# Kernel optimization log

Hardware: AMD Instinct MI355X
Metric: run time of the kernel (lower is better)

The kernel has to match this reference:

```python
import jax, jax.numpy as jnp
import numpy as np

CHUNKS = 4      # number of segments along in_features
QMAX = 127.0    # int8 symmetric fake quantization
EPS = 1e-8


def fake_quantize(t):
    """Per-tensor symmetric int8 fake quantization with amax scaling (STE-friendly)."""
    amax = jnp.max(jnp.abs(t))
    scale = jnp.maximum(amax / QMAX, EPS)
    q = jnp.clip(jnp.round(t / scale), -QMAX, QMAX) * scale
    # straight-through estimator: identity gradient through the quantizer
    return t + jax.lax.stop_gradient(q - t)


def setup_inputs() -> dict:
    key = jax.random.key(0)
    kx, kw = jax.random.split(key)
    N, K, O = 4096, 4096, 4096  # tokens (B*S), in_features, out_features
    x = jax.random.normal(kx, (N, K), dtype=jnp.float32)
    weight = jax.random.normal(kw, (O, K), dtype=jnp.float32)
    return {"x": x, "weight": weight}


def reference(x, weight):
    # seg_mode='input': split x and weight along in_features into CHUNKS equal chunks,
    # fake-quantize each chunk independently (per-chunk amax scale), run per-chunk
    # GEMMs y_i = fq(x_i) @ fq(w_i)^T and sum over chunks. No bias in 'input' mode.
    N, K = x.shape
    O = weight.shape[0]
    cs = K // CHUNKS
    xc = x.reshape(N, CHUNKS, cs)       # [N, C, cs]
    wc = weight.reshape(O, CHUNKS, cs)  # [O, C, cs]
    fq_chunks = jax.vmap(fake_quantize, in_axes=1, out_axes=1)  # independent amax per chunk
    xq = fq_chunks(xc)
    wq = fq_chunks(wc)
    # sum of per-chunk matmuls == contraction over (chunk, within-chunk) axes
    return jnp.einsum('nck,ock->no', xq, wq)
```

## Files before the change

### kernel.cpp

```cpp
#include <hip/hip_runtime.h>
#include <hip/hip_bf16.h>


constexpr int NDIM = 4096;
constexpr int TOTAL4 = (NDIM * NDIM) / 4;

typedef int i32x4 __attribute__((ext_vector_type(4)));

__global__ __launch_bounds__(256) void amax_kernel(
    const float* __restrict__ x, const float* __restrict__ w,
    unsigned int* __restrict__ amax) {
  const int t = threadIdx.x;
  const int c = blockIdx.x & 3;
  float mx = 0.f, mw = 0.f;
  const float4* x4 = (const float4*)x;
  const float4* w4 = (const float4*)w;
  const int stride = 1024 * 256;
  for (int i = blockIdx.x * 256 + t; i < TOTAL4; i += stride) {
    float4 v = x4[i];
    mx = fmaxf(mx, fmaxf(fmaxf(fabsf(v.x), fabsf(v.y)),
                         fmaxf(fabsf(v.z), fabsf(v.w))));
    float4 u = w4[i];
    mw = fmaxf(mw, fmaxf(fmaxf(fabsf(u.x), fabsf(u.y)),
                         fmaxf(fabsf(u.z), fabsf(u.w))));
  }
  __shared__ float r0[256], r1[256];
  r0[t] = mx; r1[t] = mw;
  __syncthreads();
  for (int off = 128; off; off >>= 1) {
    if (t < off) {
      r0[t] = fmaxf(r0[t], r0[t + off]);
      r1[t] = fmaxf(r1[t], r1[t + off]);
    }
    __syncthreads();
  }
  if (t == 0) {
    atomicMax(&amax[c],     __float_as_uint(r0[0]));
    atomicMax(&amax[4 + c], __float_as_uint(r1[0]));
  }
}

__device__ __forceinline__ signed char quant1(float v, float s) {
  float r = rintf(v / s);
  r = fminf(fmaxf(r, -127.f), 127.f);
  return (signed char)(int)r;
}

__global__ __launch_bounds__(256) void quant_kernel(
    const float* __restrict__ x, const float* __restrict__ w,
    const unsigned int* __restrict__ amax,
    signed char* __restrict__ qx, signed char* __restrict__ qw) {
  const int t = threadIdx.x;
  const int c = blockIdx.x & 3;
  const float sx = fmaxf(__uint_as_float(amax[c])     / 127.0f, 1e-8f);
  const float sw = fmaxf(__uint_as_float(amax[4 + c]) / 127.0f, 1e-8f);
  const float4* x4 = (const float4*)x;
  const float4* w4 = (const float4*)w;
  char4* qx4 = (char4*)qx;
  char4* qw4 = (char4*)qw;
  const int stride = 1024 * 256;
  for (int i = blockIdx.x * 256 + t; i < TOTAL4; i += stride) {
    float4 v = x4[i];
    char4 q;
    q.x = quant1(v.x, sx); q.y = quant1(v.y, sx);
    q.z = quant1(v.z, sx); q.w = quant1(v.w, sx);
    qx4[i] = q;
    float4 u = w4[i];
    char4 p;
    p.x = quant1(u.x, sw); p.y = quant1(u.y, sw);
    p.z = quant1(u.z, sw); p.w = quant1(u.w, sw);
    qw4[i] = p;
  }
}

__device__ __forceinline__ void async16(const void* g, void* l) {
  __builtin_amdgcn_global_load_lds(
      (const __attribute__((address_space(1))) void*)g,
      (__attribute__((address_space(3))) void*)l, 16, 0, 0);
}

__global__ __launch_bounds__(256, 2) void gemm_i8_kernel(
    const signed char* __restrict__ qx, const signed char* __restrict__ qw,
    const unsigned int* __restrict__ amax, float* __restrict__ out) {
  __shared__ __align__(1024) signed char lds_a[3][8192];
  __shared__ __align__(1024) signed char lds_b[3][8192];

  const int t = threadIdx.x;
  const int lane = t & 63;
  const int wave = t >> 6;
  const int brow = blockIdx.y * 128;
  const int bcol = blockIdx.x * 128;
  const int wr = wave >> 1;
  const int wc = wave & 1;

  const float s0 = fmaxf(__uint_as_float(amax[0]) / 127.0f, 1e-8f) *
                   fmaxf(__uint_as_float(amax[4]) / 127.0f, 1e-8f);
  const float s1 = fmaxf(__uint_as_float(amax[1]) / 127.0f, 1e-8f) *
                   fmaxf(__uint_as_float(amax[5]) / 127.0f, 1e-8f);
  const float s2 = fmaxf(__uint_as_float(amax[2]) / 127.0f, 1e-8f) *
                   fmaxf(__uint_as_float(amax[6]) / 127.0f, 1e-8f);
  const float s3 = fmaxf(__uint_as_float(amax[3]) / 127.0f, 1e-8f) *
                   fmaxf(__uint_as_float(amax[7]) / 127.0f, 1e-8f);
  asm volatile("s_waitcnt vmcnt(0)" ::: "memory");
  __builtin_amdgcn_sched_barrier(0);

  const int ar0 = wave * 16 + (lane >> 2);
  const int ar1 = ar0 + 64;
  const int sl = lane & 3;
  const signed char* gax0 = qx + (size_t)(brow + ar0) * NDIM + ((sl ^ ((ar0 >> 1) & 3)) << 4);
  const signed char* gax1 = qx + (size_t)(brow + ar1) * NDIM + ((sl ^ ((ar1 >> 1) & 3)) << 4);
  const signed char* gbx0 = qw + (size_t)(bcol + ar0) * NDIM + ((sl ^ ((ar0 >> 1) & 3)) << 4);
  const signed char* gbx1 = qw + (size_t)(bcol + ar1) * NDIM + ((sl ^ ((ar1 >> 1) & 3)) << 4);
  const int ldsoff = wave * 1024;

  const int ra = wr * 64 + (lane & 15);
  const int rb = wc * 64 + (lane & 15);
  const int kg = lane >> 4;
  const int offa = ra * 64 + ((kg ^ ((ra >> 1) & 3)) << 4);
  const int offb = rb * 64 + ((kg ^ ((rb >> 1) & 3)) << 4);

#define STAGE(BUFOFF, T)                                         \
  do {                                                           \
    const int kt_ = (T) * 64;                                    \
    signed char* la_ = &lds_a[0][0] + (BUFOFF) + ldsoff;         \
    signed char* lb_ = &lds_b[0][0] + (BUFOFF) + ldsoff;         \
    async16(gax0 + kt_, la_);                                    \
    async16(gax1 + kt_, la_ + 4096);                             \
    async16(gbx0 + kt_, lb_);                                    \
    async16(gbx1 + kt_, lb_ + 4096);                             \
  } while (0)

  STAGE(0, 0);
  STAGE(8192, 1);
  STAGE(16384, 2);

  i32x4 iacc[4][4];
  float facc[4][4][4];
#pragma unroll
  for (int m = 0; m < 4; ++m)
#pragma unroll
    for (int n = 0; n < 4; ++n) {
      iacc[m][n] = i32x4{0, 0, 0, 0};
#pragma unroll
      for (int j = 0; j < 4; ++j) facc[m][n][j] = 0.f;
    }

#define COMPUTE(BUFOFF)                                                 \
  do {                                                                  \
    const signed char* la_ = &lds_a[0][0] + (BUFOFF);                   \
    const signed char* lb_ = &lds_b[0][0] + (BUFOFF);                   \
    i32x4 av[4], bv[4];                                                 \
    _Pragma("unroll")                                                   \
    for (int m = 0; m < 4; ++m)                                         \
      av[m] = *(const i32x4*)&la_[offa + m * 1024];                     \
    _Pragma("unroll")                                                   \
    for (int n = 0; n < 4; ++n)                                         \
      bv[n] = *(const i32x4*)&lb_[offb + n * 1024];                     \
    __builtin_amdgcn_s_setprio(1);                                      \
    _Pragma("unroll")                                                   \
    for (int m = 0; m < 4; ++m)                                         \
      _Pragma("unroll")                                                 \
      for (int n = 0; n < 4; ++n)                                       \
        iacc[m][n] = __builtin_amdgcn_mfma_i32_16x16x64_i8(             \
            av[m], bv[n], iacc[m][n], 0, 0, 0);                         \
    __builtin_amdgcn_s_setprio(0);                                      \
  } while (0)

#define FOLD(S)                                                         \
  do {                                                                  \
    _Pragma("unroll")                                                   \
    for (int m = 0; m < 4; ++m)                                         \
      _Pragma("unroll")                                                 \
      for (int n = 0; n < 4; ++n) {                                     \
        _Pragma("unroll")                                               \
        for (int j = 0; j < 4; ++j) facc[m][n][j] += (S) * (float)iacc[m][n][j]; \
        iacc[m][n] = i32x4{0, 0, 0, 0};                                 \
      }                                                                 \
  } while (0)

#define WAITV(N) \
  asm volatile("s_waitcnt vmcnt(" #N ")" ::: "memory"); \
  __builtin_amdgcn_sched_barrier(0)
#define WAITL \
  asm volatile("s_waitcnt lgkmcnt(0)" ::: "memory"); \
  __builtin_amdgcn_sched_barrier(0)
#define BAR \
  __builtin_amdgcn_s_barrier(); \
  __builtin_amdgcn_sched_barrier(0)

  int bufoff = 0;
#pragma unroll 1
  for (int tt = 0; tt < 62; ++tt) {
    WAITV(8); BAR;
    COMPUTE(bufoff);
    WAITL; BAR;
    if (tt < 61) STAGE(bufoff, tt + 3);
    if ((tt & 15) == 15) {
      const int ci = tt >> 4;
      FOLD(ci == 0 ? s0 : ci == 1 ? s1 : s2);
    }
    bufoff = (bufoff == 16384) ? 0 : bufoff + 8192;
  }
  WAITV(4); BAR;
  COMPUTE(16384);
  WAITL; BAR;
  WAITV(0); BAR;
  COMPUTE(0);
  FOLD(s3);

  const int orow = brow + wr * 64 + (lane >> 4) * 4;
  const int ocol = bcol + wc * 64 + (lane & 15);
#pragma unroll
  for (int m = 0; m < 4; ++m)
#pragma unroll
    for (int n = 0; n < 4; ++n)
#pragma unroll
      for (int j = 0; j < 4; ++j)
        out[(size_t)(orow + m * 16 + j) * NDIM + (ocol + n * 16)] = facc[m][n][j];
#undef STAGE
#undef COMPUTE
#undef FOLD
#undef WAITV
#undef WAITL
#undef BAR
}

extern "C" void kernel_launch(void* const* d_in, const int* in_sizes, int n_in,
                              void* d_out, int out_size, void* d_ws, size_t ws_size,
                              hipStream_t stream) {
  const float* x = (const float*)d_in[0];
  const float* w = (const float*)d_in[1];
  float* out = (float*)d_out;

  unsigned int* amax = (unsigned int*)d_ws;
  signed char* qx = (signed char*)d_ws + 256;
  signed char* qw = qx + (size_t)NDIM * NDIM;

  hipMemsetAsync(d_ws, 0, 256, stream);
  amax_kernel<<<1024, 256, 0, stream>>>(x, w, amax);
  quant_kernel<<<1024, 256, 0, stream>>>(x, w, amax, qx, qw);
  dim3 grid(NDIM / 128, NDIM / 128);
  gemm_i8_kernel<<<grid, 256, 0, stream>>>(qx, qw, amax, out);
}
```

Baseline: 163.9 us.

## Use K=128 tiles with double buffering instead of K=64 triple buffering

The int8 GEMM main loop now stages 128-wide K tiles, eight async global-to-LDS loads per thread per stage, into two 16 KB buffers per operand instead of three 8 KB ones. Each compute step issues two halves of MFMAs over the wider tile, halving the number of barrier and wait rounds. The LDS swizzle is reworked to an 8-way XOR for the 128-byte rows. In exchange, prefetch depth drops from three stages to two, which may expose more global latency. Per-thread load counts and vmcnt thresholds also change.

```diff
diff --git a/kernel.cpp b/kernel.cpp
--- a/kernel.cpp
+++ b/kernel.cpp
@@ -82,8 +82,8 @@
 __global__ __launch_bounds__(256, 2) void gemm_i8_kernel(
     const signed char* __restrict__ qx, const signed char* __restrict__ qw,
     const unsigned int* __restrict__ amax, float* __restrict__ out) {
-  __shared__ __align__(1024) signed char lds_a[3][8192];
-  __shared__ __align__(1024) signed char lds_b[3][8192];
+  __shared__ __align__(1024) signed char lds_a[2][16384];
+  __shared__ __align__(1024) signed char lds_b[2][16384];
 
   const int t = threadIdx.x;
   const int lane = t & 63;
@@ -104,35 +104,35 @@
   asm volatile("s_waitcnt vmcnt(0)" ::: "memory");
   __builtin_amdgcn_sched_barrier(0);
 
-  const int ar0 = wave * 16 + (lane >> 2);
-  const int ar1 = ar0 + 64;
-  const int sl = lane & 3;
-  const signed char* gax0 = qx + (size_t)(brow + ar0) * NDIM + ((sl ^ ((ar0 >> 1) & 3)) << 4);
-  const signed char* gax1 = qx + (size_t)(brow + ar1) * NDIM + ((sl ^ ((ar1 >> 1) & 3)) << 4);
-  const signed char* gbx0 = qw + (size_t)(bcol + ar0) * NDIM + ((sl ^ ((ar0 >> 1) & 3)) << 4);
-  const signed char* gbx1 = qw + (size_t)(bcol + ar1) * NDIM + ((sl ^ ((ar1 >> 1) & 3)) << 4);
-  const int ldsoff = wave * 1024;
-
-  const int ra = wr * 64 + (lane & 15);
-  const int rb = wc * 64 + (lane & 15);
+  const int srow = t >> 3;
+  const int scol = (((t & 7) ^ (srow & 7)) << 4);
+  const signed char* gA = qx + (size_t)(brow + srow) * NDIM + scol;
+  const signed char* gB = qw + (size_t)(bcol + srow) * NDIM + scol;
+  signed char* laW = &lds_a[0][0] + wave * 1024;
+  signed char* lbW = &lds_b[0][0] + wave * 1024;
+
   const int kg = lane >> 4;
-  const int offa = ra * 64 + ((kg ^ ((ra >> 1) & 3)) << 4);
-  const int offb = rb * 64 + ((kg ^ ((rb >> 1) & 3)) << 4);
-
-#define STAGE(BUFOFF, T)                                         \
-  do {                                                           \
-    const int kt_ = (T) * 64;                                    \
-    signed char* la_ = &lds_a[0][0] + (BUFOFF) + ldsoff;         \
-    signed char* lb_ = &lds_b[0][0] + (BUFOFF) + ldsoff;         \
-    async16(gax0 + kt_, la_);                                    \
-    async16(gax1 + kt_, la_ + 4096);                             \
-    async16(gbx0 + kt_, lb_);                                    \
-    async16(gbx1 + kt_, lb_ + 4096);                             \
+  const int l7 = lane & 7;
+  const int sk0 = ((kg) ^ l7) << 4;
+  const int sk1 = ((4 + kg) ^ l7) << 4;
+  const int rba = (wr * 64 + (lane & 15)) * 128;
+  const int rbb = (wc * 64 + (lane & 15)) * 128;
+
+#define STAGE(BUFOFF, T)                                              \
+  do {                                                                \
+    const size_t kt_ = (size_t)(T) * 128;                             \
+    async16(gA + kt_,                  laW + (BUFOFF));               \
+    async16(gA + kt_ + 32u * NDIM,     laW + (BUFOFF) + 4096);        \
+    async16(gA + kt_ + 64u * NDIM,     laW + (BUFOFF) + 8192);        \
+    async16(gA + kt_ + 96u * NDIM,     laW + (BUFOFF) + 12288);       \
+    async16(gB + kt_,                  lbW + (BUFOFF));               \
+    async16(gB + kt_ + 32u * NDIM,     lbW + (BUFOFF) + 4096);        \
+    async16(gB + kt_ + 64u * NDIM,     lbW + (BUFOFF) + 8192);        \
+    async16(gB + kt_ + 96u * NDIM,     lbW + (BUFOFF) + 12288);       \
   } while (0)
 
   STAGE(0, 0);
-  STAGE(8192, 1);
-  STAGE(16384, 2);
+  STAGE(16384, 1);
 
   i32x4 iacc[4][4];
   float facc[4][4][4];
@@ -145,17 +145,15 @@
       for (int j = 0; j < 4; ++j) facc[m][n][j] = 0.f;
     }
 
-#define COMPUTE(BUFOFF)                                                 \
+#define HALF(LA, LB, SK)                                                \
   do {                                                                  \
-    const signed char* la_ = &lds_a[0][0] + (BUFOFF);                   \
-    const signed char* lb_ = &lds_b[0][0] + (BUFOFF);                   \
     i32x4 av[4], bv[4];                                                 \
     _Pragma("unroll")                                                   \
     for (int m = 0; m < 4; ++m)                                         \
-      av[m] = *(const i32x4*)&la_[offa + m * 1024];                     \
+      av[m] = *(const i32x4*)&(LA)[rba + m * 2048 + (SK)];              \
     _Pragma("unroll")                                                   \
     for (int n = 0; n < 4; ++n)                                         \
-      bv[n] = *(const i32x4*)&lb_[offb + n * 1024];                     \
+      bv[n] = *(const i32x4*)&(LB)[rbb + n * 2048 + (SK)];              \
     __builtin_amdgcn_s_setprio(1);                                      \
     _Pragma("unroll")                                                   \
     for (int m = 0; m < 4; ++m)                                         \
@@ -164,6 +162,14 @@
         iacc[m][n] = __builtin_amdgcn_mfma_i32_16x16x64_i8(             \
             av[m], bv[n], iacc[m][n], 0, 0, 0);                         \
     __builtin_amdgcn_s_setprio(0);                                      \
+  } while (0)
+
+#define COMPUTE(BUFOFF)                                                 \
+  do {                                                                  \
+    const signed char* la_ = &lds_a[0][0] + (BUFOFF);                   \
+    const signed char* lb_ = &lds_b[0][0] + (BUFOFF);                   \
+    HALF(la_, lb_, sk0);                                                \
+    HALF(la_, lb_, sk1);                                                \
   } while (0)
 
 #define FOLD(S)                                                         \
@@ -188,24 +194,26 @@
   __builtin_amdgcn_s_barrier(); \
   __builtin_amdgcn_sched_barrier(0)
 
-  int bufoff = 0;
 #pragma unroll 1
-  for (int tt = 0; tt < 62; ++tt) {
+  for (int it = 0; it < 15; ++it) {
     WAITV(8); BAR;
-    COMPUTE(bufoff);
+    COMPUTE(0);
     WAITL; BAR;
-    if (tt < 61) STAGE(bufoff, tt + 3);
-    if ((tt & 15) == 15) {
-      const int ci = tt >> 4;
+    STAGE(0, 2 * it + 2);
+    WAITV(8); BAR;
+    COMPUTE(16384);
+    WAITL; BAR;
+    STAGE(16384, 2 * it + 3);
+    if ((it & 3) == 3) {
+      const int ci = it >> 2;
       FOLD(ci == 0 ? s0 : ci == 1 ? s1 : s2);
     }
-    bufoff = (bufoff == 16384) ? 0 : bufoff + 8192;
-  }
-  WAITV(4); BAR;
-  COMPUTE(16384);
+  }
+  WAITV(8); BAR;
+  COMPUTE(0);
   WAITL; BAR;
   WAITV(0); BAR;
-  COMPUTE(0);
+  COMPUTE(16384);
   FOLD(s3);
 
   const int orow = brow + wr * 64 + (lane >> 4) * 4;
@@ -218,6 +226,7 @@
       for (int j = 0; j < 4; ++j)
         out[(size_t)(orow + m * 16 + j) * NDIM + (ocol + n * 16)] = facc[m][n][j];
 #undef STAGE
+#undef HALF
 #undef COMPUTE
 #undef FOLD
 #undef WAITV
```

Result: faster. 144.9 us, median of 2 (-11.6%).

## Enlarge GEMM tile to 256x128 with 8 waves and interleaved half-step pipeline

Applied to the files above, without the earlier changes.

The int8 GEMM kernel now uses 512-thread blocks computing 256x128 output tiles, so each B tile loaded from memory is reused across twice as many rows. It switches to a 4-deep LDS ring and splits each k-step into two halves, issuing the async loads for A and B between the MFMA groups so data movement overlaps with compute. It also adds more barriers per step and raises LDS use to 96 KB per block, which limits occupancy to one block per CU. The A/B tile addressing is reworked to match the new staging layout.

```diff
diff --git a/kernel.cpp b/kernel.cpp
--- a/kernel.cpp
+++ b/kernel.cpp
@@ -79,16 +79,16 @@
       (__attribute__((address_space(3))) void*)l, 16, 0, 0);
 }
 
-__global__ __launch_bounds__(256, 2) void gemm_i8_kernel(
+__global__ __launch_bounds__(512, 1) void gemm_i8_kernel(
     const signed char* __restrict__ qx, const signed char* __restrict__ qw,
     const unsigned int* __restrict__ amax, float* __restrict__ out) {
-  __shared__ __align__(1024) signed char lds_a[3][8192];
-  __shared__ __align__(1024) signed char lds_b[3][8192];
+  __shared__ __align__(1024) signed char lds_a[4][16384];
+  __shared__ __align__(1024) signed char lds_b[4][8192];
 
   const int t = threadIdx.x;
   const int lane = t & 63;
   const int wave = t >> 6;
-  const int brow = blockIdx.y * 128;
+  const int brow = blockIdx.y * 256;
   const int bcol = blockIdx.x * 128;
   const int wr = wave >> 1;
   const int wc = wave & 1;
@@ -104,35 +104,43 @@
   asm volatile("s_waitcnt vmcnt(0)" ::: "memory");
   __builtin_amdgcn_sched_barrier(0);
 
-  const int ar0 = wave * 16 + (lane >> 2);
-  const int ar1 = ar0 + 64;
-  const int sl = lane & 3;
-  const signed char* gax0 = qx + (size_t)(brow + ar0) * NDIM + ((sl ^ ((ar0 >> 1) & 3)) << 4);
-  const signed char* gax1 = qx + (size_t)(brow + ar1) * NDIM + ((sl ^ ((ar1 >> 1) & 3)) << 4);
-  const signed char* gbx0 = qw + (size_t)(bcol + ar0) * NDIM + ((sl ^ ((ar0 >> 1) & 3)) << 4);
-  const signed char* gbx1 = qw + (size_t)(bcol + ar1) * NDIM + ((sl ^ ((ar1 >> 1) & 3)) << 4);
-  const int ldsoff = wave * 1024;
-
-  const int ra = wr * 64 + (lane & 15);
-  const int rb = wc * 64 + (lane & 15);
+  const int sr = t >> 2;
+  const int scol = (((t & 3) ^ ((t >> 3) & 3)) << 4);
+  const signed char* gA = qx + (size_t)(brow + sr) * NDIM + scol;
+  const signed char* gB = qw + (size_t)(bcol + sr) * NDIM + scol;
+
   const int kg = lane >> 4;
-  const int offa = ra * 64 + ((kg ^ ((ra >> 1) & 3)) << 4);
-  const int offb = rb * 64 + ((kg ^ ((rb >> 1) & 3)) << 4);
-
-#define STAGE(BUFOFF, T)                                         \
-  do {                                                           \
-    const int kt_ = (T) * 64;                                    \
-    signed char* la_ = &lds_a[0][0] + (BUFOFF) + ldsoff;         \
-    signed char* lb_ = &lds_b[0][0] + (BUFOFF) + ldsoff;         \
-    async16(gax0 + kt_, la_);                                    \
-    async16(gax1 + kt_, la_ + 4096);                             \
-    async16(gbx0 + kt_, lb_);                                    \
-    async16(gbx1 + kt_, lb_ + 4096);                             \
-  } while (0)
-
-  STAGE(0, 0);
-  STAGE(8192, 1);
-  STAGE(16384, 2);
+  const int l15 = lane & 15;
+  const int ksl = ((kg ^ ((l15 >> 1) & 3)) << 4);
+  const int offa = (wr * 64 + l15) * 64 + ksl;
+  const int offb = (wc * 64 + l15) * 64 + ksl;
+
+#define STAGE_A(BUF, H)                                                  \
+  do {                                                                   \
+    const size_t kb_ = (size_t)(H) * 64;                                 \
+    async16(gA + kb_,                &lds_a[BUF][0] + t * 16);           \
+    async16(gA + kb_ + 128u * NDIM,  &lds_a[BUF][8192] + t * 16);        \
+  } while (0)
+#define STAGE_B(BUF, H)                                                  \
+  do {                                                                   \
+    const size_t kb_ = (size_t)(H) * 64;                                 \
+    async16(gB + kb_, &lds_b[BUF][0] + t * 16);                          \
+  } while (0)
+
+#define LDA(BUF, M) (*(const i32x4*)&lds_a[BUF][offa + (M) * 1024])
+#define LDB(BUF, N) (*(const i32x4*)&lds_b[BUF][offb + (N) * 1024])
+#define MM(AV, BV, M, N) \
+  iacc[M][N] = __builtin_amdgcn_mfma_i32_16x16x64_i8((AV), (BV), iacc[M][N], 0, 0, 0)
+
+#define WAITL \
+  asm volatile("s_waitcnt lgkmcnt(0)" ::: "memory"); \
+  __builtin_amdgcn_sched_barrier(0)
+#define BAR \
+  __builtin_amdgcn_s_barrier(); \
+  __builtin_amdgcn_sched_barrier(0)
+
+  STAGE_A(0, 0); STAGE_B(0, 0);
+  STAGE_A(1, 1); STAGE_B(1, 1);
 
   i32x4 iacc[4][4];
   float facc[4][4][4];
@@ -145,26 +153,9 @@
       for (int j = 0; j < 4; ++j) facc[m][n][j] = 0.f;
     }
 
-#define COMPUTE(BUFOFF)                                                 \
-  do {                                                                  \
-    const signed char* la_ = &lds_a[0][0] + (BUFOFF);                   \
-    const signed char* lb_ = &lds_b[0][0] + (BUFOFF);                   \
-    i32x4 av[4], bv[4];                                                 \
-    _Pragma("unroll")                                                   \
-    for (int m = 0; m < 4; ++m)                                         \
-      av[m] = *(const i32x4*)&la_[offa + m * 1024];                     \
-    _Pragma("unroll")                                                   \
-    for (int n = 0; n < 4; ++n)                                         \
-      bv[n] = *(const i32x4*)&lb_[offb + n * 1024];                     \
-    __builtin_amdgcn_s_setprio(1);                                      \
-    _Pragma("unroll")                                                   \
-    for (int m = 0; m < 4; ++m)                                         \
-      _Pragma("unroll")                                                 \
-      for (int n = 0; n < 4; ++n)                                       \
-        iacc[m][n] = __builtin_amdgcn_mfma_i32_16x16x64_i8(             \
-            av[m], bv[n], iacc[m][n], 0, 0, 0);                         \
-    __builtin_amdgcn_s_setprio(0);                                      \
-  } while (0)
+  asm volatile("s_waitcnt vmcnt(3)" ::: "memory");
+  __builtin_amdgcn_sched_barrier(0);
+  BAR;
 
 #define FOLD(S)                                                         \
   do {                                                                  \
@@ -178,38 +169,56 @@
       }                                                                 \
   } while (0)
 
-#define WAITV(N) \
-  asm volatile("s_waitcnt vmcnt(" #N ")" ::: "memory"); \
-  __builtin_amdgcn_sched_barrier(0)
-#define WAITL \
-  asm volatile("s_waitcnt lgkmcnt(0)" ::: "memory"); \
-  __builtin_amdgcn_sched_barrier(0)
-#define BAR \
-  __builtin_amdgcn_s_barrier(); \
-  __builtin_amdgcn_sched_barrier(0)
-
-  int bufoff = 0;
+#define HALF(BUF, H2, EN, VM)                                           \
+  do {                                                                  \
+    i32x4 av0 = LDA(BUF, 0), av1 = LDA(BUF, 1);                         \
+    i32x4 av2 = LDA(BUF, 2), av3 = LDA(BUF, 3);                         \
+    i32x4 bv0 = LDB(BUF, 0), bv1 = LDB(BUF, 1);                         \
+    if (EN) STAGE_A(((BUF) + 2) & 3, H2);                               \
+    BAR;                                                                \
+    WAITL;                                                              \
+    __builtin_amdgcn_s_setprio(1);                                      \
+    MM(av0, bv0, 0, 0); MM(av1, bv0, 1, 0);                             \
+    MM(av2, bv0, 2, 0); MM(av3, bv0, 3, 0);                             \
+    MM(av0, bv1, 0, 1); MM(av1, bv1, 1, 1);                             \
+    MM(av2, bv1, 2, 1); MM(av3, bv1, 3, 1);                             \
+    __builtin_amdgcn_s_setprio(0);                                      \
+    BAR;                                                                \
+    i32x4 bv2 = LDB(BUF, 2), bv3 = LDB(BUF, 3);                         \
+    if (EN) STAGE_B(((BUF) + 2) & 3, H2);                               \
+    BAR;                                                                \
+    WAITL;                                                              \
+    __builtin_amdgcn_s_setprio(1);                                      \
+    MM(av0, bv2, 0, 2); MM(av1, bv2, 1, 2);                             \
+    MM(av2, bv2, 2, 2); MM(av3, bv2, 3, 2);                             \
+    MM(av0, bv3, 0, 3); MM(av1, bv3, 1, 3);                             \
+    MM(av2, bv3, 2, 3); MM(av3, bv3, 3, 3);                             \
+    __builtin_amdgcn_s_setprio(0);                                      \
+    asm volatile(VM ::: "memory");                                      \
+    __builtin_amdgcn_sched_barrier(0);                                  \
+    BAR;                                                                \
+  } while (0)
+
 #pragma unroll 1
-  for (int tt = 0; tt < 62; ++tt) {
-    WAITV(8); BAR;
-    COMPUTE(bufoff);
-    WAITL; BAR;
-    if (tt < 61) STAGE(bufoff, tt + 3);
-    if ((tt & 15) == 15) {
-      const int ci = tt >> 4;
+  for (int hh = 0; hh < 15; ++hh) {
+    const int h = hh * 4;
+    HALF(0, h + 2, 1, "s_waitcnt vmcnt(3)");
+    HALF(1, h + 3, 1, "s_waitcnt vmcnt(3)");
+    HALF(2, h + 4, 1, "s_waitcnt vmcnt(3)");
+    HALF(3, h + 5, 1, "s_waitcnt vmcnt(3)");
+    if ((hh & 3) == 3) {
+      const int ci = hh >> 2;
       FOLD(ci == 0 ? s0 : ci == 1 ? s1 : s2);
     }
-    bufoff = (bufoff == 16384) ? 0 : bufoff + 8192;
-  }
-  WAITV(4); BAR;
-  COMPUTE(16384);
-  WAITL; BAR;
-  WAITV(0); BAR;
-  COMPUTE(0);
+  }
+  HALF(0, 62, 1, "s_waitcnt vmcnt(3)");
+  HALF(1, 63, 1, "s_waitcnt vmcnt(3)");
+  HALF(2, 0, 0, "s_waitcnt vmcnt(0)");
+  HALF(3, 0, 0, "s_nop 0");
   FOLD(s3);
 
   const int orow = brow + wr * 64 + (lane >> 4) * 4;
-  const int ocol = bcol + wc * 64 + (lane & 15);
+  const int ocol = bcol + wc * 64 + l15;
 #pragma unroll
   for (int m = 0; m < 4; ++m)
 #pragma unroll
@@ -217,12 +226,15 @@
 #pragma unroll
       for (int j = 0; j < 4; ++j)
         out[(size_t)(orow + m * 16 + j) * NDIM + (ocol + n * 16)] = facc[m][n][j];
-#undef STAGE
-#undef COMPUTE
-#undef FOLD
-#undef WAITV
+#undef STAGE_A
+#undef STAGE_B
+#undef LDA
+#undef LDB
+#undef MM
 #undef WAITL
 #undef BAR
+#undef FOLD
+#undef HALF
 }
 
 extern "C" void kernel_launch(void* const* d_in, const int* in_sizes, int n_in,
@@ -239,6 +251,6 @@
   hipMemsetAsync(d_ws, 0, 256, stream);
   amax_kernel<<<1024, 256, 0, stream>>>(x, w, amax);
   quant_kernel<<<1024, 256, 0, stream>>>(x, w, amax, qx, qw);
-  dim3 grid(NDIM / 128, NDIM / 128);
-  gemm_i8_kernel<<<grid, 256, 0, stream>>>(qx, qw, amax, out);
-}
+  dim3 grid(NDIM / 128, NDIM / 256);
+  gemm_i8_kernel<<<grid, 512, 0, stream>>>(qx, qw, amax, out);
+}
```

New measurement: 174.1 us. +6.2%, slower.
